# Kernel tuning notes

Measured on AMD Instinct MI355X. Metric: run time of the kernel, lower is better.

## Reference

```python
import jax, jax.numpy as jnp
import numpy as np
import math

FACTOR = 5

def setup_inputs() -> dict:
    key = jax.random.key(0)
    kq, kk, kv = jax.random.split(key, 3)
    B, L, H, D = 2, 4096, 8, 64
    queries = jax.random.normal(kq, (B, L, H, D), dtype=jnp.float32)
    keys = jax.random.normal(kk, (B, L, H, D), dtype=jnp.float32)
    values = jax.random.normal(kv, (B, L, H, D), dtype=jnp.float32)
    attn_mask = jnp.ones((B, L), dtype=jnp.int32)
    return {"queries": queries, "keys": keys, "values": values, "attn_mask": attn_mask}

def reference(queries, keys, values, attn_mask):
    B, L_Q, H, D = queries.shape
    L_K = keys.shape[1]
    # [B, L, H, D] -> [B, H, L, D]
    Q = jnp.transpose(queries, (0, 2, 1, 3))
    K = jnp.transpose(keys, (0, 2, 1, 3))
    V = jnp.transpose(values, (0, 2, 1, 3))

    U_part = max(min(FACTOR * int(math.ceil(math.log(max(L_K, 1)))), L_K), 1)
    u = max(min(FACTOR * int(math.ceil(math.log(max(L_Q, 1)))), L_Q), 1)

    # random key sampling per query (torch.randint replaced by fixed jax key)
    idx = jax.random.randint(jax.random.key(1), (L_Q, U_part), 0, L_K)  # [L_Q, S]
    K_sample = K[:, :, idx, :]  # [B, H, L_Q, S, D]  (irregular gather)
    Q_K_sample = jnp.einsum('bhqd,bhqsd->bhqs', Q, K_sample)  # [B, H, L_Q, S]

    # sparsity measure M = max - mean(full-length normalization L_K as in source)
    M = Q_K_sample.max(axis=-1) - Q_K_sample.sum(axis=-1) / L_K  # [B, H, L_Q]
    _, M_top = jax.lax.top_k(M, u)  # [B, H, u]

    Q_reduce = jnp.take_along_axis(Q, M_top[..., None], axis=2)  # [B, H, u, D]
    scale = 1.0 / math.sqrt(D)
    scores = jnp.einsum('bhud,bhkd->bhuk', Q_reduce, K) * scale  # [B, H, u, L_K]

    mask = attn_mask[:, None, None, :]  # [B,1,1,L_K]
    scores = jnp.where(mask == 0, -jnp.inf, scores)

    A = jax.nn.softmax(scores, axis=-1)  # dropout p=0 -> identity
    context = jnp.einsum('bhuk,bhkd->bhud', A, V)  # [B, H, u, D]
    return jnp.transpose(context, (0, 2, 1, 3))  # [B, u, H, D]
```

## Files before the change

kernel.cpp:

```cpp
#include <hip/hip_runtime.h>
#include <math.h>

#define JAX_PARTITIONABLE 1

constexpr int Bc = 2, Lc = 4096, Hc = 8, Dc = 64;
constexpr int BHc = Bc * Hc;
constexpr int Uc = 45;
constexpr int NSc = 45;

typedef float vfloat4 __attribute__((ext_vector_type(4)));

struct TF2 { unsigned a, b; };

__host__ __device__ constexpr unsigned rotl32(unsigned v, int n) {
  return (v << n) | (v >> (32 - n));
}

__host__ __device__ constexpr TF2 tf2(unsigned k0, unsigned k1, unsigned x0, unsigned x1) {
  unsigned ks2 = k0 ^ k1 ^ 0x1BD11BDAu;
  x0 += k0; x1 += k1;
  x0 += x1; x1 = rotl32(x1, 13); x1 ^= x0;
  x0 += x1; x1 = rotl32(x1, 15); x1 ^= x0;
  x0 += x1; x1 = rotl32(x1, 26); x1 ^= x0;
  x0 += x1; x1 = rotl32(x1, 6);  x1 ^= x0;
  x0 += k1; x1 += ks2 + 1u;
  x0 += x1; x1 = rotl32(x1, 17); x1 ^= x0;
  x0 += x1; x1 = rotl32(x1, 29); x1 ^= x0;
  x0 += x1; x1 = rotl32(x1, 16); x1 ^= x0;
  x0 += x1; x1 = rotl32(x1, 24); x1 ^= x0;
  x0 += ks2; x1 += k0 + 2u;
  x0 += x1; x1 = rotl32(x1, 13); x1 ^= x0;
  x0 += x1; x1 = rotl32(x1, 15); x1 ^= x0;
  x0 += x1; x1 = rotl32(x1, 26); x1 ^= x0;
  x0 += x1; x1 = rotl32(x1, 6);  x1 ^= x0;
  x0 += k0; x1 += k1 + 3u;
  x0 += x1; x1 = rotl32(x1, 17); x1 ^= x0;
  x0 += x1; x1 = rotl32(x1, 29); x1 ^= x0;
  x0 += x1; x1 = rotl32(x1, 16); x1 ^= x0;
  x0 += x1; x1 = rotl32(x1, 24); x1 ^= x0;
  x0 += k1; x1 += ks2 + 4u;
  x0 += x1; x1 = rotl32(x1, 13); x1 ^= x0;
  x0 += x1; x1 = rotl32(x1, 15); x1 ^= x0;
  x0 += x1; x1 = rotl32(x1, 26); x1 ^= x0;
  x0 += x1; x1 = rotl32(x1, 6);  x1 ^= x0;
  x0 += ks2; x1 += k0 + 5u;
  return TF2{x0, x1};
}

template <int CTRL>
__device__ __forceinline__ float dpp_add(float x) {
  int t = __builtin_amdgcn_update_dpp(0, __float_as_int(x), CTRL, 0xF, 0xF, false);
  return x + __int_as_float(t);
}
template <int CTRL>
__device__ __forceinline__ float dpp_idf(float x) {
  int t = __builtin_amdgcn_update_dpp(__float_as_int(x), __float_as_int(x), CTRL, 0xF, 0xF, false);
  return __int_as_float(t);
}
__device__ __forceinline__ float wave_max_bcast(float x) {
  x = fmaxf(x, dpp_idf<0x111>(x));
  x = fmaxf(x, dpp_idf<0x112>(x));
  x = fmaxf(x, dpp_idf<0x114>(x));
  x = fmaxf(x, dpp_idf<0x118>(x));
  x = fmaxf(x, dpp_idf<0x142>(x));
  x = fmaxf(x, dpp_idf<0x143>(x));
  return __int_as_float(__builtin_amdgcn_readlane(__float_as_int(x), 63));
}
__device__ __forceinline__ float wave_sum_bcast(float x) {
  x = dpp_add<0x111>(x);
  x = dpp_add<0x112>(x);
  x = dpp_add<0x114>(x);
  x = dpp_add<0x118>(x);
  x = dpp_add<0x142>(x);
  x = dpp_add<0x143>(x);
  return __int_as_float(__builtin_amdgcn_readlane(__float_as_int(x), 63));
}

__device__ __forceinline__ float dot4_acc(float4 q, float4 k, float a) {
  a = fmaf(q.x, k.x, a);
  a = fmaf(q.y, k.y, a);
  a = fmaf(q.z, k.z, a);
  a = fmaf(q.w, k.w, a);
  return a;
}

__global__ __launch_bounds__(256) void k_scoreM(const float* __restrict__ Q, const float* __restrict__ K,
                                                float* __restrict__ M) {
  __shared__ int sidx[720];
  int tid = threadIdx.x;
  int bx = blockIdx.x;
  int bh = bx & 15;
  int qblk = bx >> 4;
  int b = bh >> 3, h = bh & 7;
  int lane16 = tid & 15, qloc = tid >> 4;
  int q = qblk * 16 + qloc;
  constexpr TF2 kb = tf2(0u, 1u, 0u, 1u);
  for (int e = tid; e < 720; e += 256) {
    TF2 r = tf2(kb.a, kb.b, 0u, (unsigned)(qblk * 720 + e));
    sidx[e] = (int)((r.a ^ r.b) & 4095u);
  }
  __syncthreads();
  const vfloat4* Q4 = (const vfloat4*)Q;
  const vfloat4* K4 = (const vfloat4*)K;
  vfloat4 qr = Q4[((b * Lc + q) * Hc + h) * 16 + lane16];
  int kbase = (b * Lc * Hc + h) * 16 + lane16;
  const int* ip = sidx + qloc * NSc;
  float mx = -INFINITY, sm = 0.f;
  #pragma unroll
  for (int s0 = 0; s0 < NSc; s0 += 5) {
    int kk[5];
    #pragma unroll
    for (int i = 0; i < 5; ++i) kk[i] = ip[s0 + i];
    vfloat4 kv[5];
    #pragma unroll
    for (int i = 0; i < 5; ++i) kv[i] = __builtin_nontemporal_load(&K4[kbase + kk[i] * (Hc * 16)]);
    #pragma unroll
    for (int i = 0; i < 5; ++i) {
      float p = fmaf(qr[0], kv[i][0], fmaf(qr[1], kv[i][1], fmaf(qr[2], kv[i][2], qr[3] * kv[i][3])));
      p = dpp_add<0x111>(p);
      p = dpp_add<0x112>(p);
      p = dpp_add<0x114>(p);
      p = dpp_add<0x118>(p);
      mx = fmaxf(mx, p);
      sm += p;
    }
  }
  if (lane16 == 15) M[bh * Lc + q] = mx - sm * (1.0f / Lc);
}

__global__ __launch_bounds__(256) void k_topk(const float* __restrict__ M, const float* __restrict__ Q,
                                              int* __restrict__ topk, float* __restrict__ qg) {
  __shared__ unsigned su[Lc];
  __shared__ int hist[256];
  __shared__ int sfx[257];
  __shared__ unsigned s_prefix;
  __shared__ int s_r;
  __shared__ int n_gt, n_eq;
  __shared__ unsigned cu[64];
  __shared__ int cidx[64];
  __shared__ int eqi[64];
  __shared__ int srank[Uc];
  int bh = blockIdx.x, tid = threadIdx.x;
  int b = bh >> 3, h = bh & 7;
  const float* m = M + bh * Lc;
  for (int e = tid; e < Lc; e += 256) {
    unsigned bb = __float_as_uint(m[e]);
    su[e] = (bb & 0x80000000u) ? ~bb : (bb | 0x80000000u);
  }
  if (tid == 0) { s_r = Uc; s_prefix = 0u; n_gt = 0; n_eq = 0; }
  __syncthreads();
  #pragma unroll
  for (int p = 0; p < 4; ++p) {
    int shift = 24 - 8 * p;
    hist[tid] = 0;
    __syncthreads();
    unsigned pref = s_prefix;
    unsigned hmask = (p == 0) ? 0u : (0xFFFFFFFFu << (shift + 8));
    for (int e = tid; e < Lc; e += 256) {
      unsigned u = su[e];
      if ((u & hmask) == pref) atomicAdd(&hist[(u >> shift) & 255u], 1);
    }
    __syncthreads();
    sfx[tid] = hist[tid];
    __syncthreads();
    for (int off = 1; off < 256; off <<= 1) {
      int v = (tid + off < 256) ? sfx[tid + off] : 0;
      __syncthreads();
      sfx[tid] += v;
      __syncthreads();
    }
    int r = s_r;
    __syncthreads();
    int above = (tid < 255) ? sfx[tid + 1] : 0;
    if (sfx[tid] >= r && above < r) {
      s_r = r - above;
      s_prefix = pref | ((unsigned)tid << shift);
    }
    __syncthreads();
  }
  unsigned T = s_prefix;
  int rf = s_r;
  for (int e = tid; e < Lc; e += 256) {
    unsigned u = su[e];
    if (u > T) {
      int p = atomicAdd(&n_gt, 1);
      cu[p] = u; cidx[p] = e;
    } else if (u == T) {
      int p = atomicAdd(&n_eq, 1);
      if (p < 64) eqi[p] = e;
    }
  }
  __syncthreads();
  int ne = n_eq < 64 ? n_eq : 64;
  if (tid < ne) {
    int myi = eqi[tid];
    int rank = 0;
    for (int j = 0; j < ne; ++j) rank += (eqi[j] < myi);
    if (rank < rf) {
      int p = atomicAdd(&n_gt, 1);
      cu[p] = T; cidx[p] = myi;
    }
  }
  __syncthreads();
  if (tid < Uc) {
    unsigned mu = cu[tid]; int mi = cidx[tid];
    int rank = 0;
    for (int j = 0; j < Uc; ++j) {
      unsigned ju = cu[j]; int ji = cidx[j];
      rank += (ju > mu) || (ju == mu && ji < mi);
    }
    topk[bh * Uc + rank] = mi;
    srank[rank] = mi;
  }
  __syncthreads();
  const float4* Q4 = (const float4*)Q;
  float4* qg4 = (float4*)qg;
  for (int e = tid; e < Uc * 16; e += 256) {
    int t = e >> 4, dq = e & 15;
    qg4[bh * Uc * 16 + e] = Q4[((b * Lc + srank[t]) * Hc + h) * 16 + dq];
  }
}

template<int NC>
__global__ __launch_bounds__(256) void k_attn(const float* __restrict__ qg, const float* __restrict__ K,
                                              const float* __restrict__ V, const int* __restrict__ amask,
                                              float* __restrict__ pO, float* __restrict__ pM,
                                              float* __restrict__ pL) {
  constexpr int CH = Lc / NC;
  constexpr int TG = 256 / CH;
  constexpr int SCW = CH + 4;
  int chunk = blockIdx.x, bh = blockIdx.y;
  int b = bh >> 3, h = bh & 7;
  int tid = threadIdx.x;
  __shared__ __align__(16) float qs[Uc * 64];
  __shared__ __align__(16) float sc[48][SCW];
  {
    const float4* qg4 = (const float4*)qg;
    float4* qs4w = (float4*)qs;
    for (int e = tid; e < Uc * 16; e += 256) qs4w[e] = qg4[bh * Uc * 16 + e];
  }
  for (int e = tid; e < 3 * SCW; e += 256) sc[45 + e / SCW][e % SCW] = 0.f;
  __syncthreads();
  {
    int k = tid % CH, tg = tid / CH;
    int key = chunk * CH + k;
    const float4* K4 = (const float4*)K;
    int kb = ((b * Lc + key) * Hc + h) * 16;
    float4 kr[16];
    #pragma unroll
    for (int j = 0; j < 16; ++j) kr[j] = K4[kb + j];
    int mk = amask[b * Lc + key];
    const float4* qs4 = (const float4*)qs;
    for (int t = tg; t < Uc; t += TG) {
      float a0 = 0.f, a1 = 0.f, a2 = 0.f, a3 = 0.f;
      #pragma unroll
      for (int j = 0; j < 16; j += 4) {
        a0 = dot4_acc(qs4[t * 16 + j],     kr[j],     a0);
        a1 = dot4_acc(qs4[t * 16 + j + 1], kr[j + 1], a1);
        a2 = dot4_acc(qs4[t * 16 + j + 2], kr[j + 2], a2);
        a3 = dot4_acc(qs4[t * 16 + j + 3], kr[j + 3], a3);
      }
      float acc = (a0 + a1) + (a2 + a3);
      sc[t][k] = mk ? acc * 0.125f : -INFINITY;
    }
  }
  __syncthreads();
  {
    int w = tid >> 6, lane = tid & 63;
    for (int t = w; t < Uc; t += 4) {
      float x = sc[t][lane];
      float ml = wave_max_bcast(x);
      float p = (ml != -INFINITY) ? __expf(x - ml) : 0.f;
      sc[t][lane] = p;
      float ls = wave_sum_bcast(p);
      if (lane == 0) {
        pM[(bh * NC + chunk) * Uc + t] = ml;
        pL[(bh * NC + chunk) * Uc + t] = ls;
      }
    }
  }
  __syncthreads();
  {
    int ty = tid >> 4, tx = tid & 15;
    float4 o0 = {0.f, 0.f, 0.f, 0.f};
    float4 o1 = {0.f, 0.f, 0.f, 0.f};
    float4 o2 = {0.f, 0.f, 0.f, 0.f};
    const float4* V4 = (const float4*)V;
    const float4* s0 = (const float4*)&sc[ty][0];
    const float4* s1 = (const float4*)&sc[ty + 16][0];
    const float4* s2 = (const float4*)&sc[ty + 32][0];
    int vbase = (b * Lc + chunk * CH) * (Hc * 16) + h * 16 + tx;
    #pragma unroll 2
    for (int kq = 0; kq < CH / 4; ++kq) {
      float4 p0 = s0[kq], p1 = s1[kq], p2 = s2[kq];
      float4 va = V4[vbase + (4 * kq + 0) * (Hc * 16)];
      float4 vb = V4[vbase + (4 * kq + 1) * (Hc * 16)];
      float4 vc = V4[vbase + (4 * kq + 2) * (Hc * 16)];
      float4 vd = V4[vbase + (4 * kq + 3) * (Hc * 16)];
      o0.x = fmaf(p0.x, va.x, o0.x); o0.y = fmaf(p0.x, va.y, o0.y); o0.z = fmaf(p0.x, va.z, o0.z); o0.w = fmaf(p0.x, va.w, o0.w);
      o1.x = fmaf(p1.x, va.x, o1.x); o1.y = fmaf(p1.x, va.y, o1.y); o1.z = fmaf(p1.x, va.z, o1.z); o1.w = fmaf(p1.x, va.w, o1.w);
      o2.x = fmaf(p2.x, va.x, o2.x); o2.y = fmaf(p2.x, va.y, o2.y); o2.z = fmaf(p2.x, va.z, o2.z); o2.w = fmaf(p2.x, va.w, o2.w);
      o0.x = fmaf(p0.y, vb.x, o0.x); o0.y = fmaf(p0.y, vb.y, o0.y); o0.z = fmaf(p0.y, vb.z, o0.z); o0.w = fmaf(p0.y, vb.w, o0.w);
      o1.x = fmaf(p1.y, vb.x, o1.x); o1.y = fmaf(p1.y, vb.y, o1.y); o1.z = fmaf(p1.y, vb.z, o1.z); o1.w = fmaf(p1.y, vb.w, o1.w);
      o2.x = fmaf(p2.y, vb.x, o2.x); o2.y = fmaf(p2.y, vb.y, o2.y); o2.z = fmaf(p2.y, vb.z, o2.z); o2.w = fmaf(p2.y, vb.w, o2.w);
      o0.x = fmaf(p0.z, vc.x, o0.x); o0.y = fmaf(p0.z, vc.y, o0.y); o0.z = fmaf(p0.z, vc.z, o0.z); o0.w = fmaf(p0.z, vc.w, o0.w);
      o1.x = fmaf(p1.z, vc.x, o1.x); o1.y = fmaf(p1.z, vc.y, o1.y); o1.z = fmaf(p1.z, vc.z, o1.z); o1.w = fmaf(p1.z, vc.w, o1.w);
      o2.x = fmaf(p2.z, vc.x, o2.x); o2.y = fmaf(p2.z, vc.y, o2.y); o2.z = fmaf(p2.z, vc.z, o2.z); o2.w = fmaf(p2.z, vc.w, o2.w);
      o0.x = fmaf(p0.w, vd.x, o0.x); o0.y = fmaf(p0.w, vd.y, o0.y); o0.z = fmaf(p0.w, vd.z, o0.z); o0.w = fmaf(p0.w, vd.w, o0.w);
      o1.x = fmaf(p1.w, vd.x, o1.x); o1.y = fmaf(p1.w, vd.y, o1.y); o1.z = fmaf(p1.w, vd.z, o1.z); o1.w = fmaf(p1.w, vd.w, o1.w);
      o2.x = fmaf(p2.w, vd.x, o2.x); o2.y = fmaf(p2.w, vd.y, o2.y); o2.z = fmaf(p2.w, vd.z, o2.z); o2.w = fmaf(p2.w, vd.w, o2.w);
    }
    float4* pO4 = (float4*)pO;
    int obase = ((bh * NC + chunk) * Uc) * 16 + tx;
    pO4[obase + ty * 16] = o0;
    pO4[obase + (ty + 16) * 16] = o1;
    if (ty < 13) pO4[obase + (ty + 32) * 16] = o2;
  }
}

template<int NC>
__global__ __launch_bounds__(256) void k_merge(const float* __restrict__ pO, const float* __restrict__ pM,
                                               const float* __restrict__ pL, float* __restrict__ out) {
  int f = blockIdx.x * 256 + threadIdx.x;
  int d = f & 63, h = (f >> 6) & 7;
  int bt = f >> 9;
  int t = bt % Uc, b = bt / Uc;
  int bh = b * 8 + h;
  float m = -INFINITY;
  for (int c = 0; c < NC; ++c) m = fmaxf(m, pM[(bh * NC + c) * Uc + t]);
  float den = 0.f, num = 0.f;
  for (int c = 0; c < NC; ++c) {
    float mc = pM[(bh * NC + c) * Uc + t];
    float wgt = (mc == -INFINITY) ? 0.f : __expf(mc - m);
    den += wgt * pL[(bh * NC + c) * Uc + t];
    num += wgt * pO[((bh * NC + c) * Uc + t) * 64 + d];
  }
  out[f] = num / den;
}

extern "C" void kernel_launch(void* const* d_in, const int* in_sizes, int n_in,
                              void* d_out, int out_size, void* d_ws, size_t ws_size,
                              hipStream_t stream) {
  const float* Q = (const float*)d_in[0];
  const float* K = (const float*)d_in[1];
  const float* V = (const float*)d_in[2];
  const int* amask = (const int*)d_in[3];
  float* out = (float*)d_out;
  char* ws = (char*)d_ws;
  float* M    = (float*)(ws + 0x000000);
  int*   topk = (int*)(ws + 0x040000);
  float* qg   = (float*)(ws + 0x041000);
  float* pM   = (float*)(ws + 0x070000);
  size_t need64 = 0x70000UL + 64UL * 190080UL;
  size_t need32 = 0x70000UL + 32UL * 190080UL;
  int NC = ws_size >= need64 ? 64 : (ws_size >= need32 ? 32 : 16);
  float* pL = pM + 16 * NC * Uc;
  float* pO = pL + 16 * NC * Uc;

  k_scoreM<<<4096, 256, 0, stream>>>(Q, K, M);
  k_topk<<<BHc, 256, 0, stream>>>(M, Q, topk, qg);
  if (NC == 64) {
    k_attn<64><<<dim3(64, BHc), 256, 0, stream>>>(qg, K, V, amask, pO, pM, pL);
    k_merge<64><<<180, 256, 0, stream>>>(pO, pM, pL, out);
  } else if (NC == 32) {
    k_attn<32><<<dim3(32, BHc), 256, 0, stream>>>(qg, K, V, amask, pO, pM, pL);
    k_merge<32><<<180, 256, 0, stream>>>(pO, pM, pL, out);
  } else {
    k_attn<16><<<dim3(16, BHc), 256, 0, stream>>>(qg, K, V, amask, pO, pM, pL);
    k_merge<16><<<180, 256, 0, stream>>>(pO, pM, pL, out);
  }
}
```

Baseline: 180.2 us.

## Precompute sample indices in a separate kernel and widen per-thread work in scoreM

```diff
diff --git a/kernel.cpp b/kernel.cpp
--- a/kernel.cpp
+++ b/kernel.cpp
@@ -83,49 +83,72 @@
   a = fmaf(q.w, k.w, a);
   return a;
 }
+__device__ __forceinline__ float dot4v(vfloat4 q, vfloat4 k, float a) {
+  a = fmaf(q[0], k[0], a);
+  a = fmaf(q[1], k[1], a);
+  a = fmaf(q[2], k[2], a);
+  a = fmaf(q[3], k[3], a);
+  return a;
+}
+
+__global__ __launch_bounds__(256) void k_genidx(int* __restrict__ gidx) {
+  unsigned g = blockIdx.x * 256u + threadIdx.x;
+  constexpr TF2 kb = tf2(0u, 1u, 0u, 1u);
+  TF2 r = tf2(kb.a, kb.b, 0u, g);
+  gidx[g] = (int)((r.a ^ r.b) & 4095u);
+}
 
 __global__ __launch_bounds__(256) void k_scoreM(const float* __restrict__ Q, const float* __restrict__ K,
-                                                float* __restrict__ M) {
-  __shared__ int sidx[720];
+                                                const int* __restrict__ gidx, float* __restrict__ M) {
+  __shared__ int sidx[64 * NSc];
   int tid = threadIdx.x;
   int bx = blockIdx.x;
   int bh = bx & 15;
   int qblk = bx >> 4;
   int b = bh >> 3, h = bh & 7;
-  int lane16 = tid & 15, qloc = tid >> 4;
-  int q = qblk * 16 + qloc;
-  constexpr TF2 kb = tf2(0u, 1u, 0u, 1u);
-  for (int e = tid; e < 720; e += 256) {
-    TF2 r = tf2(kb.a, kb.b, 0u, (unsigned)(qblk * 720 + e));
-    sidx[e] = (int)((r.a ^ r.b) & 4095u);
+  int sec = tid & 3, qloc = tid >> 2;
+  int q = qblk * 64 + qloc;
+  {
+    const int4* g4 = (const int4*)(gidx + qblk * (64 * NSc));
+    int4* s4 = (int4*)sidx;
+    for (int e = tid; e < 720; e += 256) s4[e] = g4[e];
   }
   __syncthreads();
   const vfloat4* Q4 = (const vfloat4*)Q;
   const vfloat4* K4 = (const vfloat4*)K;
-  vfloat4 qr = Q4[((b * Lc + q) * Hc + h) * 16 + lane16];
-  int kbase = (b * Lc * Hc + h) * 16 + lane16;
+  vfloat4 qr[4];
+  int qb4 = ((b * Lc + q) * Hc + h) * 16 + sec;
+  #pragma unroll
+  for (int j = 0; j < 4; ++j) qr[j] = Q4[qb4 + 4 * j];
+  int kbase = (b * Lc * Hc + h) * 16 + sec;
   const int* ip = sidx + qloc * NSc;
   float mx = -INFINITY, sm = 0.f;
   #pragma unroll
-  for (int s0 = 0; s0 < NSc; s0 += 5) {
-    int kk[5];
+  for (int s0 = 0; s0 < NSc; s0 += 3) {
+    int kk[3];
     #pragma unroll
-    for (int i = 0; i < 5; ++i) kk[i] = ip[s0 + i];
-    vfloat4 kv[5];
+    for (int i = 0; i < 3; ++i) kk[i] = ip[s0 + i];
+    vfloat4 kv[3][4];
     #pragma unroll
-    for (int i = 0; i < 5; ++i) kv[i] = __builtin_nontemporal_load(&K4[kbase + kk[i] * (Hc * 16)]);
+    for (int i = 0; i < 3; ++i) {
+      #pragma unroll
+      for (int j = 0; j < 4; ++j)
+        kv[i][j] = __builtin_nontemporal_load(&K4[kbase + kk[i] * (Hc * 16) + 4 * j]);
+    }
     #pragma unroll
-    for (int i = 0; i < 5; ++i) {
-      float p = fmaf(qr[0], kv[i][0], fmaf(qr[1], kv[i][1], fmaf(qr[2], kv[i][2], qr[3] * kv[i][3])));
+    for (int i = 0; i < 3; ++i) {
+      float a0 = dot4v(qr[0], kv[i][0], 0.f);
+      a0 = dot4v(qr[1], kv[i][1], a0);
+      float a1 = dot4v(qr[2], kv[i][2], 0.f);
+      a1 = dot4v(qr[3], kv[i][3], a1);
+      float p = a0 + a1;
       p = dpp_add<0x111>(p);
       p = dpp_add<0x112>(p);
-      p = dpp_add<0x114>(p);
-      p = dpp_add<0x118>(p);
       mx = fmaxf(mx, p);
       sm += p;
     }
   }
-  if (lane16 == 15) M[bh * Lc + q] = mx - sm * (1.0f / Lc);
+  if (sec == 3) M[bh * Lc + q] = mx - sm * (1.0f / Lc);
 }
 
 __global__ __launch_bounds__(256) void k_topk(const float* __restrict__ M, const float* __restrict__ Q,
@@ -350,14 +373,16 @@
   float* M    = (float*)(ws + 0x000000);
   int*   topk = (int*)(ws + 0x040000);
   float* qg   = (float*)(ws + 0x041000);
-  float* pM   = (float*)(ws + 0x070000);
-  size_t need64 = 0x70000UL + 64UL * 190080UL;
-  size_t need32 = 0x70000UL + 32UL * 190080UL;
+  int*   gidx = (int*)(ws + 0x070000);
+  float* pM   = (float*)(ws + 0x130000);
+  size_t need64 = 0x130000UL + 64UL * 190080UL;
+  size_t need32 = 0x130000UL + 32UL * 190080UL;
   int NC = ws_size >= need64 ? 64 : (ws_size >= need32 ? 32 : 16);
   float* pL = pM + 16 * NC * Uc;
   float* pO = pL + 16 * NC * Uc;
 
-  k_scoreM<<<4096, 256, 0, stream>>>(Q, K, M);
+  k_genidx<<<720, 256, 0, stream>>>(gidx);
+  k_scoreM<<<1024, 256, 0, stream>>>(Q, K, gidx, M);
   k_topk<<<BHc, 256, 0, stream>>>(M, Q, topk, qg);
   if (NC == 64) {
     k_attn<64><<<dim3(64, BHc), 256, 0, stream>>>(qg, K, V, amask, pO, pM, pL);
```

Result: slower. 239.9 us (+33.1%).

## Fuse top-k into scoring and merge into attention via last-block atomic counters

Applied to the files above, without the earlier changes.

```diff
diff --git a/kernel.cpp b/kernel.cpp
--- a/kernel.cpp
+++ b/kernel.cpp
@@ -84,9 +84,31 @@
   return a;
 }
 
-__global__ __launch_bounds__(256) void k_scoreM(const float* __restrict__ Q, const float* __restrict__ K,
-                                                float* __restrict__ M) {
-  __shared__ int sidx[720];
+struct TopkSh {
+  unsigned su[Lc];
+  int hist[256];
+  int sfx[257];
+  unsigned s_prefix;
+  int s_r;
+  int n_gt, n_eq;
+  unsigned cu[64];
+  int cidx[64];
+  int eqi[64];
+  int srank[Uc];
+};
+union ShA {
+  int sidx[720];
+  TopkSh tk;
+};
+
+__global__ __launch_bounds__(256) void k_scoreM_topk(const float* __restrict__ Q,
+                                                     const float* __restrict__ K,
+                                                     float* __restrict__ M,
+                                                     int* __restrict__ cnt,
+                                                     int* __restrict__ topk,
+                                                     float* __restrict__ qg) {
+  __shared__ ShA sh;
+  __shared__ int s_go;
   int tid = threadIdx.x;
   int bx = blockIdx.x;
   int bh = bx & 15;
@@ -97,135 +119,133 @@
   constexpr TF2 kb = tf2(0u, 1u, 0u, 1u);
   for (int e = tid; e < 720; e += 256) {
     TF2 r = tf2(kb.a, kb.b, 0u, (unsigned)(qblk * 720 + e));
-    sidx[e] = (int)((r.a ^ r.b) & 4095u);
-  }
-  __syncthreads();
-  const vfloat4* Q4 = (const vfloat4*)Q;
-  const vfloat4* K4 = (const vfloat4*)K;
-  vfloat4 qr = Q4[((b * Lc + q) * Hc + h) * 16 + lane16];
-  int kbase = (b * Lc * Hc + h) * 16 + lane16;
-  const int* ip = sidx + qloc * NSc;
-  float mx = -INFINITY, sm = 0.f;
-  #pragma unroll
-  for (int s0 = 0; s0 < NSc; s0 += 5) {
-    int kk[5];
+    sh.sidx[e] = (int)((r.a ^ r.b) & 4095u);
+  }
+  __syncthreads();
+  {
+    const vfloat4* Q4 = (const vfloat4*)Q;
+    const vfloat4* K4 = (const vfloat4*)K;
+    vfloat4 qr = Q4[((b * Lc + q) * Hc + h) * 16 + lane16];
+    int kbase = (b * Lc * Hc + h) * 16 + lane16;
+    const int* ip = sh.sidx + qloc * NSc;
+    float mx = -INFINITY, sm = 0.f;
     #pragma unroll
-    for (int i = 0; i < 5; ++i) kk[i] = ip[s0 + i];
-    vfloat4 kv[5];
-    #pragma unroll
-    for (int i = 0; i < 5; ++i) kv[i] = __builtin_nontemporal_load(&K4[kbase + kk[i] * (Hc * 16)]);
-    #pragma unroll
-    for (int i = 0; i < 5; ++i) {
-      float p = fmaf(qr[0], kv[i][0], fmaf(qr[1], kv[i][1], fmaf(qr[2], kv[i][2], qr[3] * kv[i][3])));
-      p = dpp_add<0x111>(p);
-      p = dpp_add<0x112>(p);
-      p = dpp_add<0x114>(p);
-      p = dpp_add<0x118>(p);
-      mx = fmaxf(mx, p);
-      sm += p;
-    }
-  }
-  if (lane16 == 15) M[bh * Lc + q] = mx - sm * (1.0f / Lc);
-}
-
-__global__ __launch_bounds__(256) void k_topk(const float* __restrict__ M, const float* __restrict__ Q,
-                                              int* __restrict__ topk, float* __restrict__ qg) {
-  __shared__ unsigned su[Lc];
-  __shared__ int hist[256];
-  __shared__ int sfx[257];
-  __shared__ unsigned s_prefix;
-  __shared__ int s_r;
-  __shared__ int n_gt, n_eq;
-  __shared__ unsigned cu[64];
-  __shared__ int cidx[64];
-  __shared__ int eqi[64];
-  __shared__ int srank[Uc];
-  int bh = blockIdx.x, tid = threadIdx.x;
-  int b = bh >> 3, h = bh & 7;
+    for (int s0 = 0; s0 < NSc; s0 += 5) {
+      int kk[5];
+      #pragma unroll
+      for (int i = 0; i < 5; ++i) kk[i] = ip[s0 + i];
+      vfloat4 kv[5];
+      #pragma unroll
+      for (int i = 0; i < 5; ++i) kv[i] = __builtin_nontemporal_load(&K4[kbase + kk[i] * (Hc * 16)]);
+      #pragma unroll
+      for (int i = 0; i < 5; ++i) {
+        float p = fmaf(qr[0], kv[i][0], fmaf(qr[1], kv[i][1], fmaf(qr[2], kv[i][2], qr[3] * kv[i][3])));
+        p = dpp_add<0x111>(p);
+        p = dpp_add<0x112>(p);
+        p = dpp_add<0x114>(p);
+        p = dpp_add<0x118>(p);
+        mx = fmaxf(mx, p);
+        sm += p;
+      }
+    }
+    if (lane16 == 15) M[bh * Lc + q] = mx - sm * (1.0f / Lc);
+  }
+  __syncthreads();
+  if (tid == 0) {
+    __threadfence();
+    int old = atomicAdd(&cnt[bh], 1);
+    s_go = (old == 255) ? 1 : 0;
+  }
+  __syncthreads();
+  if (!s_go) return;
+  if (tid == 0) __threadfence();
+  __syncthreads();
+
   const float* m = M + bh * Lc;
   for (int e = tid; e < Lc; e += 256) {
     unsigned bb = __float_as_uint(m[e]);
-    su[e] = (bb & 0x80000000u) ? ~bb : (bb | 0x80000000u);
-  }
-  if (tid == 0) { s_r = Uc; s_prefix = 0u; n_gt = 0; n_eq = 0; }
+    sh.tk.su[e] = (bb & 0x80000000u) ? ~bb : (bb | 0x80000000u);
+  }
+  if (tid == 0) { sh.tk.s_r = Uc; sh.tk.s_prefix = 0u; sh.tk.n_gt = 0; sh.tk.n_eq = 0; }
   __syncthreads();
   #pragma unroll
   for (int p = 0; p < 4; ++p) {
     int shift = 24 - 8 * p;
-    hist[tid] = 0;
+    sh.tk.hist[tid] = 0;
     __syncthreads();
-    unsigned pref = s_prefix;
+    unsigned pref = sh.tk.s_prefix;
     unsigned hmask = (p == 0) ? 0u : (0xFFFFFFFFu << (shift + 8));
     for (int e = tid; e < Lc; e += 256) {
-      unsigned u = su[e];
-      if ((u & hmask) == pref) atomicAdd(&hist[(u >> shift) & 255u], 1);
+      unsigned u = sh.tk.su[e];
+      if ((u & hmask) == pref) atomicAdd(&sh.tk.hist[(u >> shift) & 255u], 1);
     }
     __syncthreads();
-    sfx[tid] = hist[tid];
+    sh.tk.sfx[tid] = sh.tk.hist[tid];
     __syncthreads();
     for (int off = 1; off < 256; off <<= 1) {
-      int v = (tid + off < 256) ? sfx[tid + off] : 0;
+      int v = (tid + off < 256) ? sh.tk.sfx[tid + off] : 0;
       __syncthreads();
-      sfx[tid] += v;
+      sh.tk.sfx[tid] += v;
       __syncthreads();
     }
-    int r = s_r;
+    int r = sh.tk.s_r;
     __syncthreads();
-    int above = (tid < 255) ? sfx[tid + 1] : 0;
-    if (sfx[tid] >= r && above < r) {
-      s_r = r - above;
-      s_prefix = pref | ((unsigned)tid << shift);
+    int above = (tid < 255) ? sh.tk.sfx[tid + 1] : 0;
+    if (sh.tk.sfx[tid] >= r && above < r) {
+      sh.tk.s_r = r - above;
+      sh.tk.s_prefix = pref | ((unsigned)tid << shift);
     }
     __syncthreads();
   }
-  unsigned T = s_prefix;
-  int rf = s_r;
+  unsigned T = sh.tk.s_prefix;
+  int rf = sh.tk.s_r;
   for (int e = tid; e < Lc; e += 256) {
-    unsigned u = su[e];
+    unsigned u = sh.tk.su[e];
     if (u > T) {
-      int p = atomicAdd(&n_gt, 1);
-      cu[p] = u; cidx[p] = e;
+      int p = atomicAdd(&sh.tk.n_gt, 1);
+      sh.tk.cu[p] = u; sh.tk.cidx[p] = e;
     } else if (u == T) {
-      int p = atomicAdd(&n_eq, 1);
-      if (p < 64) eqi[p] = e;
-    }
-  }
-  __syncthreads();
-  int ne = n_eq < 64 ? n_eq : 64;
+      int p = atomicAdd(&sh.tk.n_eq, 1);
+      if (p < 64) sh.tk.eqi[p] = e;
+    }
+  }
+  __syncthreads();
+  int ne = sh.tk.n_eq < 64 ? sh.tk.n_eq : 64;
   if (tid < ne) {
-    int myi = eqi[tid];
+    int myi = sh.tk.eqi[tid];
     int rank = 0;
-    for (int j = 0; j < ne; ++j) rank += (eqi[j] < myi);
+    for (int j = 0; j < ne; ++j) rank += (sh.tk.eqi[j] < myi);
     if (rank < rf) {
-      int p = atomicAdd(&n_gt, 1);
-      cu[p] = T; cidx[p] = myi;
+      int p = atomicAdd(&sh.tk.n_gt, 1);
+      sh.tk.cu[p] = T; sh.tk.cidx[p] = myi;
     }
   }
   __syncthreads();
   if (tid < Uc) {
-    unsigned mu = cu[tid]; int mi = cidx[tid];
+    unsigned mu = sh.tk.cu[tid]; int mi = sh.tk.cidx[tid];
     int rank = 0;
     for (int j = 0; j < Uc; ++j) {
-      unsigned ju = cu[j]; int ji = cidx[j];
+      unsigned ju = sh.tk.cu[j]; int ji = sh.tk.cidx[j];
       rank += (ju > mu) || (ju == mu && ji < mi);
     }
     topk[bh * Uc + rank] = mi;
-    srank[rank] = mi;
+    sh.tk.srank[rank] = mi;
   }
   __syncthreads();
   const float4* Q4 = (const float4*)Q;
   float4* qg4 = (float4*)qg;
   for (int e = tid; e < Uc * 16; e += 256) {
     int t = e >> 4, dq = e & 15;
-    qg4[bh * Uc * 16 + e] = Q4[((b * Lc + srank[t]) * Hc + h) * 16 + dq];
+    qg4[bh * Uc * 16 + e] = Q4[((b * Lc + sh.tk.srank[t]) * Hc + h) * 16 + dq];
   }
 }
 
 template<int NC>
-__global__ __launch_bounds__(256) void k_attn(const float* __restrict__ qg, const float* __restrict__ K,
-                                              const float* __restrict__ V, const int* __restrict__ amask,
-                                              float* __restrict__ pO, float* __restrict__ pM,
-                                              float* __restrict__ pL) {
+__global__ __launch_bounds__(256) void k_attn_merge(const float* __restrict__ qg, const float* __restrict__ K,
+                                                    const float* __restrict__ V, const int* __restrict__ amask,
+                                                    float* __restrict__ pO, float* __restrict__ pM,
+                                                    float* __restrict__ pL, int* __restrict__ cnt,
+                                                    float* __restrict__ out) {
   constexpr int CH = Lc / NC;
   constexpr int TG = 256 / CH;
   constexpr int SCW = CH + 4;
@@ -234,6 +254,7 @@
   int tid = threadIdx.x;
   __shared__ __align__(16) float qs[Uc * 64];
   __shared__ __align__(16) float sc[48][SCW];
+  __shared__ int s_go;
   {
     const float4* qg4 = (const float4*)qg;
     float4* qs4w = (float4*)qs;
@@ -316,26 +337,34 @@
     pO4[obase + (ty + 16) * 16] = o1;
     if (ty < 13) pO4[obase + (ty + 32) * 16] = o2;
   }
-}
-
-template<int NC>
-__global__ __launch_bounds__(256) void k_merge(const float* __restrict__ pO, const float* __restrict__ pM,
-                                               const float* __restrict__ pL, float* __restrict__ out) {
-  int f = blockIdx.x * 256 + threadIdx.x;
-  int d = f & 63, h = (f >> 6) & 7;
-  int bt = f >> 9;
-  int t = bt % Uc, b = bt / Uc;
-  int bh = b * 8 + h;
-  float m = -INFINITY;
-  for (int c = 0; c < NC; ++c) m = fmaxf(m, pM[(bh * NC + c) * Uc + t]);
-  float den = 0.f, num = 0.f;
-  for (int c = 0; c < NC; ++c) {
-    float mc = pM[(bh * NC + c) * Uc + t];
-    float wgt = (mc == -INFINITY) ? 0.f : __expf(mc - m);
-    den += wgt * pL[(bh * NC + c) * Uc + t];
-    num += wgt * pO[((bh * NC + c) * Uc + t) * 64 + d];
-  }
-  out[f] = num / den;
+  __syncthreads();
+  if (tid == 0) {
+    __threadfence();
+    int old = atomicAdd(&cnt[bh], 1);
+    s_go = (old == NC - 1) ? 1 : 0;
+  }
+  __syncthreads();
+  if (!s_go) return;
+  if (tid == 0) __threadfence();
+  __syncthreads();
+  {
+    int w = tid >> 6, d = tid & 63;
+    for (int t = w; t < Uc; t += 4) {
+      int mlbase = bh * NC * Uc + t;
+      float m = -INFINITY;
+      #pragma unroll 4
+      for (int c = 0; c < NC; ++c) m = fmaxf(m, pM[mlbase + c * Uc]);
+      float den = 0.f, num = 0.f;
+      #pragma unroll 4
+      for (int c = 0; c < NC; ++c) {
+        float mc = pM[mlbase + c * Uc];
+        float wgt = (mc == -INFINITY) ? 0.f : __expf(mc - m);
+        den += wgt * pL[mlbase + c * Uc];
+        num += wgt * pO[(mlbase + c * Uc) * 64 + d];
+      }
+      out[((b * Uc + t) * Hc + h) * 64 + d] = num / den;
+    }
+  }
 }
 
 extern "C" void kernel_launch(void* const* d_in, const int* in_sizes, int n_in,
@@ -350,6 +379,8 @@
   float* M    = (float*)(ws + 0x000000);
   int*   topk = (int*)(ws + 0x040000);
   float* qg   = (float*)(ws + 0x041000);
+  int*   cntA = (int*)(ws + 0x06E000);
+  int*   cntB = cntA + 16;
   float* pM   = (float*)(ws + 0x070000);
   size_t need64 = 0x70000UL + 64UL * 190080UL;
   size_t need32 = 0x70000UL + 32UL * 190080UL;
@@ -357,16 +388,13 @@
   float* pL = pM + 16 * NC * Uc;
   float* pO = pL + 16 * NC * Uc;
 
-  k_scoreM<<<4096, 256, 0, stream>>>(Q, K, M);
-  k_topk<<<BHc, 256, 0, stream>>>(M, Q, topk, qg);
+  hipMemsetAsync(ws + 0x06E000, 0, 128, stream);
+  k_scoreM_topk<<<4096, 256, 0, stream>>>(Q, K, M, cntA, topk, qg);
   if (NC == 64) {
-    k_attn<64><<<dim3(64, BHc), 256, 0, stream>>>(qg, K, V, amask, pO, pM, pL);
-    k_merge<64><<<180, 256, 0, stream>>>(pO, pM, pL, out);
+    k_attn_merge<64><<<dim3(64, BHc), 256, 0, stream>>>(qg, K, V, amask, pO, pM, pL, cntB, out);
   } else if (NC == 32) {
-    k_attn<32><<<dim3(32, BHc), 256, 0, stream>>>(qg, K, V, amask, pO, pM, pL);
-    k_merge<32><<<180, 256, 0, stream>>>(pO, pM, pL, out);
+    k_attn_merge<32><<<dim3(32, BHc), 256, 0, stream>>>(qg, K, V, amask, pO, pM, pL, cntB, out);
   } else {
-    k_attn<16><<<dim3(16, BHc), 256, 0, stream>>>(qg, K, V, amask, pO, pM, pL);
-    k_merge<16><<<180, 256, 0, stream>>>(pO, pM, pL, out);
-  }
-}
+    k_attn_merge<16><<<dim3(16, BHc), 256, 0, stream>>>(qg, K, V, amask, pO, pM, pL, cntB, out);
+  }
+}
```

Result: slower. 494.8 us (+174.6%).
